# Kernel tuning notes

Measured on AMD Instinct MI355X. Metric: run time of the kernel, lower is better.

Reference implementation:

```python
import jax, jax.numpy as jnp
import numpy as np

N = 4096          # samples per domain
D_IN = 512        # input feature dim
H = 10            # hidden size of featurizer
D_OUT = 50        # featurizer output dim


def setup_inputs() -> dict:
    key = jax.random.key(0)
    ks = jax.random.split(key, 12)
    def lin(k, fan_in, fan_out):
        bound = 1.0 / np.sqrt(fan_in)
        kw, kb = jax.random.split(k)
        W = jax.random.uniform(kw, (fan_in, fan_out), jnp.float32, -bound, bound)
        b = jax.random.uniform(kb, (fan_out,), jnp.float32, -bound, bound)
        return W, b
    W1, b1 = lin(ks[0], D_IN, H)
    W2, b2 = lin(ks[1], H, H)
    W3, b3 = lin(ks[2], H, H)
    W4, b4 = lin(ks[3], H, D_OUT)
    Xs = jax.random.normal(ks[4], (N, D_IN), jnp.float32)
    Xt = jax.random.normal(ks[5], (N, D_IN), jnp.float32) + 0.1
    # epsilonOPT = log(rand(1) * 1e-10)
    epsilonOPT = jnp.log(jax.random.uniform(ks[6], (1,), jnp.float32) * 1e-10)
    sigmaOPT = jnp.sqrt(jnp.asarray(2.0 * 32 * 32, jnp.float32))
    sigma0OPT = jnp.sqrt(jnp.asarray(0.005, jnp.float32))
    return {"Xs": Xs, "Xt": Xt, "W1": W1, "b1": b1, "W2": W2, "b2": b2,
            "W3": W3, "b3": b3, "W4": W4, "b4": b4,
            "epsilonOPT": epsilonOPT, "sigmaOPT": sigmaOPT, "sigma0OPT": sigma0OPT}


def _pdist2(x, y):
    # squared pairwise distances, clamped at 0 (as in Pdist2)
    xn = jnp.sum(x * x, axis=1)[:, None]
    yn = jnp.sum(y * y, axis=1)[None, :]
    d = xn + yn - 2.0 * (x @ y.T)
    return jnp.maximum(d, 0.0)


def _featurize(x, W1, b1, W2, b2, W3, b3, W4, b4):
    sp = jax.nn.softplus
    h = sp(x @ W1 + b1)
    h = sp(h @ W2 + b2)
    h = sp(h @ W3 + b3)
    return h @ W4 + b4


def _deep_kernel(Dd, Do, ep, sigma, sigma0):
    # (1-ep)*exp(-Dd/sigma0 - Do/sigma) + ep*exp(-Do/sigma)   (L=1)
    e_org = jnp.exp(-Do / sigma)
    return (1.0 - ep) * jnp.exp(-Dd / sigma0) * e_org + ep * e_org


def reference(Xs, Xt, W1, b1, W2, b2, W3, b3, W4, b4, epsilonOPT, sigmaOPT, sigma0OPT):
    n = Xs.shape[0]
    Fea_org = jnp.concatenate([Xs, Xt], axis=0)
    Fea = _featurize(Fea_org, W1, b1, W2, b2, W3, b3, W4, b4)

    ep = jax.nn.sigmoid(epsilonOPT)[0]
    sigma = sigmaOPT ** 2
    sigma0 = sigma0OPT ** 2

    X, Y = Fea[:n], Fea[n:]
    Xo, Yo = Fea_org[:n], Fea_org[n:]

    Kx = _deep_kernel(_pdist2(X, X), _pdist2(Xo, Xo), ep, sigma, sigma0)
    Ky = _deep_kernel(_pdist2(Y, Y), _pdist2(Yo, Yo), ep, sigma, sigma0)
    Kxy = _deep_kernel(_pdist2(X, Y), _pdist2(Xo, Yo), ep, sigma, sigma0)

    nx = n
    ny = Fea.shape[0] - n
    # unbiased estimator with use_1sample_U=True
    xx = (jnp.sum(Kx) - jnp.trace(Kx)) / (nx * (nx - 1))
    yy = (jnp.sum(Ky) - jnp.trace(Ky)) / (ny * (ny - 1))
    xy = (jnp.sum(Kxy) - jnp.trace(Kxy)) / (nx * (ny - 1))
    mmd2 = xx - 2.0 * xy + yy
    return mmd2
```

## Files before the change

### kernel.cpp

```cpp
#include <hip/hip_runtime.h>
#include <math.h>

#define NHALF 4096
#define NTOT  8192
#define DIN   512
#define DFR   50
#define FPS   160
#define BM    128
#define NBI   64
#define NTRI  2080
#define T64STRIDE 524288
#define KCSTRIDE  65536

typedef short short8 __attribute__((ext_vector_type(8)));
typedef float f32x4 __attribute__((ext_vector_type(4)));

__device__ __forceinline__ float softplus_f(float x) {
    return fmaxf(x, 0.f) + log1pf(expf(-fabsf(x)));
}

__device__ __forceinline__ unsigned cvt_pk_bf16(float lo, float hi) {
    unsigned r;
    asm("v_cvt_pk_bf16_f32 %0, %1, %2" : "=v"(r) : "v"(lo), "v"(hi));
    return r;
}

__device__ __forceinline__ unsigned short bf16_rne(float v) {
    return (unsigned short)(cvt_pk_bf16(v, 0.f) & 0xffffu);
}

__device__ __forceinline__ float bf16_to_f(unsigned short s) {
    union { unsigned u; float f; } c;
    c.u = (unsigned)s << 16;
    return c.f;
}

__device__ __forceinline__ void gload_lds16(const void* g, void* l) {
    __builtin_amdgcn_global_load_lds(
        (const __attribute__((address_space(1))) void*)g,
        (__attribute__((address_space(3))) void*)l, 16, 0, 0);
}

__global__ __launch_bounds__(256) void featurize_kernel(
    const float* __restrict__ Xs, const float* __restrict__ Xt,
    const float* __restrict__ W1, const float* __restrict__ b1,
    const float* __restrict__ W2, const float* __restrict__ b2,
    const float* __restrict__ W3, const float* __restrict__ b3,
    const float* __restrict__ W4, const float* __restrict__ b4,
    const float* __restrict__ sigP, const float* __restrict__ sig0P,
    unsigned short* __restrict__ FpkA, unsigned short* __restrict__ FpkB,
    float* __restrict__ normC, char* __restrict__ Xb8)
{
    __shared__ float W1L[80 * 65];
    __shared__ __align__(16) unsigned short pkA[4][FPS];
    __shared__ __align__(16) unsigned short pkB[4][FPS];
    int tid = threadIdx.x;
    for (int e = tid; e < 5120; e += 256) {
        int r = e / 10, j = e - 10 * r;
        W1L[((r & 7) * 10 + j) * 65 + (r >> 3)] = W1[e];
    }
    __syncthreads();

    int row  = (blockIdx.x * blockDim.x + tid) >> 6;
    int lane = tid & 63, wv = tid >> 6;
    float alpha8 = 64.f / sigP[0];
    float beta   = 64.f / sig0P[0];
    const float* src = (row < NHALF) ? (Xs + (size_t)row * DIN)
                                     : (Xt + (size_t)(row - NHALF) * DIN);
    float4 v0 = ((const float4*)src)[lane * 2];
    float4 v1 = ((const float4*)src)[lane * 2 + 1];
    float x[8] = {v0.x, v0.y, v0.z, v0.w, v1.x, v1.y, v1.z, v1.w};

    float z[8];
#pragma unroll
    for (int t = 0; t < 8; ++t) z[t] = x[t] * alpha8;
    unsigned w0 = 0, w1 = 0;
    w0 = __builtin_amdgcn_cvt_pk_fp8_f32(z[0], z[1], w0, false);
    w0 = __builtin_amdgcn_cvt_pk_fp8_f32(z[2], z[3], w0, true);
    w1 = __builtin_amdgcn_cvt_pk_fp8_f32(z[4], z[5], w1, false);
    w1 = __builtin_amdgcn_cvt_pk_fp8_f32(z[6], z[7], w1, true);
    float on = 0.f, qf;
    qf = __builtin_amdgcn_cvt_f32_fp8(w0, 0); on = fmaf(qf, qf, on);
    qf = __builtin_amdgcn_cvt_f32_fp8(w0, 1); on = fmaf(qf, qf, on);
    qf = __builtin_amdgcn_cvt_f32_fp8(w0, 2); on = fmaf(qf, qf, on);
    qf = __builtin_amdgcn_cvt_f32_fp8(w0, 3); on = fmaf(qf, qf, on);
    qf = __builtin_amdgcn_cvt_f32_fp8(w1, 0); on = fmaf(qf, qf, on);
    qf = __builtin_amdgcn_cvt_f32_fp8(w1, 1); on = fmaf(qf, qf, on);
    qf = __builtin_amdgcn_cvt_f32_fp8(w1, 2); on = fmaf(qf, qf, on);
    qf = __builtin_amdgcn_cvt_f32_fp8(w1, 3); on = fmaf(qf, qf, on);
    *(uint2*)(Xb8 + (lane >> 3) * T64STRIDE + (lane & 7) * KCSTRIDE
              + (size_t)row * 8) = make_uint2(w0, w1);

    float p[10];
#pragma unroll
    for (int j = 0; j < 10; ++j) p[j] = 0.f;
#pragma unroll
    for (int t = 0; t < 8; ++t) {
        float xv = x[t];
#pragma unroll
        for (int j = 0; j < 10; ++j)
            p[j] = fmaf(xv, W1L[(t * 10 + j) * 65 + lane], p[j]);
    }
#pragma unroll
    for (int m = 32; m >= 1; m >>= 1) {
#pragma unroll
        for (int j = 0; j < 10; ++j) p[j] += __shfl_xor(p[j], m, 64);
        on += __shfl_xor(on, m, 64);
    }
    int lane10 = lane % 10;
    float pown = p[0];
#pragma unroll
    for (int j = 1; j < 10; ++j) pown = (lane10 == j) ? p[j] : pown;
    float hown = softplus_f(pown + b1[lane10]);
    float h1b[10];
#pragma unroll
    for (int k = 0; k < 10; ++k) h1b[k] = __shfl(hown, k, 64);

    float a2 = b2[lane10];
#pragma unroll
    for (int k = 0; k < 10; ++k) a2 = fmaf(h1b[k], W2[k * 10 + lane10], a2);
    float h2own = softplus_f(a2);
    float h2b[10];
#pragma unroll
    for (int k = 0; k < 10; ++k) h2b[k] = __shfl(h2own, k, 64);

    float a3 = b3[lane10];
#pragma unroll
    for (int k = 0; k < 10; ++k) a3 = fmaf(h2b[k], W3[k * 10 + lane10], a3);
    float h3own = softplus_f(a3);
    float h3b[10];
#pragma unroll
    for (int k = 0; k < 10; ++k) h3b[k] = __shfl(h3own, k, 64);

    float o = 0.f;
    if (lane < DFR) {
        float a = b4[lane];
#pragma unroll
        for (int k = 0; k < 10; ++k) a = fmaf(h3b[k], W4[k * 50 + lane], a);
        o = a;
    }
    float f = o * beta;
    unsigned short hi_s = bf16_rne(f);
    unsigned short lo_s = bf16_rne(f - bf16_to_f(hi_s));
    if (lane < DFR) {
        pkA[wv][lane] = hi_s;  pkA[wv][50 + lane] = hi_s;  pkA[wv][100 + lane] = lo_s;
        pkB[wv][lane] = hi_s;  pkB[wv][50 + lane] = lo_s;  pkB[wv][100 + lane] = hi_s;
    } else if (lane < 60) {
        pkA[wv][100 + lane] = 0;
        pkB[wv][100 + lane] = 0;
    }
    __syncthreads();
    if (lane < 20)
        *(uint4*)(FpkA + (size_t)row * FPS + lane * 8) = *(const uint4*)&pkA[wv][lane * 8];
    else if (lane < 40)
        *(uint4*)(FpkB + (size_t)row * FPS + (lane - 20) * 8) = *(const uint4*)&pkB[wv][(lane - 20) * 8];

    float fn = f * f;
#pragma unroll
    for (int m = 32; m >= 1; m >>= 1) fn += __shfl_xor(fn, m, 64);
    if (lane == 0) normC[row] = (on + fn) * (1.f / 4096.f);
}

__global__ __launch_bounds__(256, 3) void pairwise_kernel(
    const char* __restrict__ Xb8,
    const unsigned short* __restrict__ FpkA,
    const unsigned short* __restrict__ FpkB,
    const float* __restrict__ normC,
    double* __restrict__ partialsC)
{
    __shared__ char smem[49152] __attribute__((aligned(128)));
    __shared__ double sredC[4];

    int bid = blockIdx.x;
    int bi = (int)((129.0 - sqrt(16641.0 - 8.0 * (double)bid)) * 0.5);
    while (NBI * (bi + 1) - (bi + 1) * bi / 2 <= bid) ++bi;
    while (NBI * bi - bi * (bi - 1) / 2 > bid) --bi;
    int bj = bi + (bid - (NBI * bi - bi * (bi - 1) / 2));

    int tid = threadIdx.x;
    int lane = tid & 63, wave = tid >> 6;
    int g = lane >> 4, l15 = lane & 15;
    int i0w = (wave >> 1) * 64;
    int j0w = (wave & 1) * 64;
    int ri = bi * BM, rj = bj * BM;

    const char* sA8 = Xb8 + wave * KCSTRIDE + (size_t)(ri + 2 * lane) * 8;
    const char* sB8 = Xb8 + wave * KCSTRIDE + (size_t)(rj + 2 * lane) * 8;
    int srow = tid >> 2;
    int schunk = (tid & 3) ^ ((srow >> 1) & 3);
    const char* fA0 = (const char*)(FpkA + (size_t)(ri + srow) * FPS) + schunk * 16;
    const char* fB0 = (const char*)(FpkB + (size_t)(rj + srow) * FPS) + schunk * 16;
    char* lwave = (char*)smem + wave * 1024;

    int xoffA = (lane >> 4) * 1024 + (i0w + l15) * 8;
    int xoffB = 8192 + (lane >> 4) * 1024 + (j0w + l15) * 8;
    int swz = (l15 >> 1) & 3;
    int offA = (i0w + l15) * 32 + (g ^ swz) * 8;
    int offB = (j0w + l15) * 32 + (g ^ swz) * 8;

    f32x4 acc[4][4];
#pragma unroll
    for (int a = 0; a < 4; ++a)
#pragma unroll
        for (int b = 0; b < 4; ++b) acc[a][b] = (f32x4){0.f, 0.f, 0.f, 0.f};

#define STAGE8(kt, buf)                                              \
    do {                                                             \
        char* ld_ = lwave + (buf) * 16384;                           \
        const char* a_ = sA8 + (kt) * T64STRIDE;                     \
        const char* b_ = sB8 + (kt) * T64STRIDE;                     \
        gload_lds16(a_,              ld_);                           \
        gload_lds16(a_ + 4 * KCSTRIDE, ld_ + 4096);                  \
        gload_lds16(b_,              ld_ + 8192);                    \
        gload_lds16(b_ + 4 * KCSTRIDE, ld_ + 12288);                 \
    } while (0)

#define STAGEF(kf, buf)                                              \
    do {                                                             \
        char* ld_ = lwave + (buf) * 16384;                           \
        const char* gA_ = fA0 + (kf) * 64;                           \
        const char* gB_ = fB0 + (kf) * 64;                           \
        gload_lds16(gA_,         ld_);                               \
        gload_lds16(gA_ + 20480, ld_ + 4096);                        \
        gload_lds16(gB_,         ld_ + 8192);                        \
        gload_lds16(gB_ + 20480, ld_ + 12288);                       \
    } while (0)

#define COMPUTE8(buf)                                                              \
    do {                                                                           \
        const char* tc_ = smem + (buf) * 16384;                                    \
        _Pragma("unroll")                                                          \
        for (int h = 0; h < 2; ++h) {                                              \
            long a8_[4], b8_[4];                                                   \
            _Pragma("unroll")                                                      \
            for (int a = 0; a < 4; ++a)                                            \
                a8_[a] = *(const long*)(tc_ + xoffA + h * 4096 + a * 128);         \
            _Pragma("unroll")                                                      \
            for (int b = 0; b < 4; ++b)                                            \
                b8_[b] = *(const long*)(tc_ + xoffB + h * 4096 + b * 128);         \
            _Pragma("unroll")                                                      \
            for (int a = 0; a < 4; ++a)                                            \
                _Pragma("unroll")                                                  \
                for (int b = 0; b < 4; ++b)                                        \
                    acc[a][b] = __builtin_amdgcn_mfma_f32_16x16x32_fp8_fp8(        \
                        a8_[a], b8_[b], acc[a][b], 0, 0, 0);                       \
        }                                                                          \
    } while (0)

#define COMPUTE16(buf)                                                             \
    do {                                                                           \
        const unsigned short* tc_ = (const unsigned short*)(smem + (buf) * 16384); \
        short8 af_[4], bf_[4];                                                     \
        _Pragma("unroll")                                                          \
        for (int a = 0; a < 4; ++a)                                                \
            af_[a] = *(const short8*)(tc_ + offA + a * 512);                       \
        _Pragma("unroll")                                                          \
        for (int b = 0; b < 4; ++b)                                                \
            bf_[b] = *(const short8*)(tc_ + 4096 + offB + b * 512);                \
        _Pragma("unroll")                                                          \
        for (int a = 0; a < 4; ++a)                                                \
            _Pragma("unroll")                                                      \
            for (int b = 0; b < 4; ++b)                                            \
                acc[a][b] = __builtin_amdgcn_mfma_f32_16x16x32_bf16(               \
                    af_[a], bf_[b], acc[a][b], 0, 0, 0);                           \
    } while (0)

#define WAITV(N) do { asm volatile("s_waitcnt vmcnt(" #N ")" ::: "memory");        \
                      __builtin_amdgcn_sched_barrier(0); } while (0)
#define BARR1    do { __builtin_amdgcn_s_barrier();                                \
                      __builtin_amdgcn_sched_barrier(0); } while (0)
#define BARR2    do { __builtin_amdgcn_sched_barrier(0);                           \
                      asm volatile("s_waitcnt lgkmcnt(0)" ::: "memory");           \
                      __builtin_amdgcn_sched_barrier(0);                           \
                      __builtin_amdgcn_s_barrier();                                \
                      __builtin_amdgcn_sched_barrier(0); } while (0)

    STAGE8(0, 0);
    STAGE8(1, 1);
    STAGE8(2, 2);

    for (int kk = 0; kk < 8; ++kk) {
        WAITV(8);
        BARR1;
        COMPUTE8(kk % 3);
        BARR2;
        int kt = kk + 3;
        if (kt < 8) STAGE8(kt, kk % 3);
        else        STAGEF(kt - 8, kk % 3);
    }
    WAITV(8); BARR1; COMPUTE16(2); BARR2; STAGEF(3, 2);
    WAITV(8); BARR1; COMPUTE16(0); BARR2; STAGEF(4, 0);
    WAITV(8); BARR1; COMPUTE16(1);
    WAITV(4); BARR1; COMPUTE16(2);
    WAITV(0); BARR1; COMPUTE16(0);

    float nci[16], ncj[4];
#pragma unroll
    for (int a = 0; a < 4; ++a)
#pragma unroll
        for (int r = 0; r < 4; ++r)
            nci[a * 4 + r] = normC[ri + i0w + 16 * a + 4 * g + r];
#pragma unroll
    for (int b = 0; b < 4; ++b)
        ncj[b] = normC[rj + j0w + 16 * b + l15];

    float sgn = ((ri < NHALF) == (rj < NHALF)) ? 1.f : -1.f;
    float wsgn = 2.f * sgn;
    const float cf = 2.f / 4096.f;

    float locf = 0.f;
#pragma unroll
    for (int a = 0; a < 4; ++a)
#pragma unroll
        for (int b = 0; b < 4; ++b)
#pragma unroll
            for (int r = 0; r < 4; ++r) {
                int gi = ri + i0w + 16 * a + 4 * g + r;
                int gj = rj + j0w + 16 * b + l15;
                float Dc = fmaxf(fmaf(-cf, acc[a][b][r], nci[a * 4 + r] + ncj[b]), 0.f);
                float K = __expf(-Dc);
                float w = (gj > gi && gj != gi + NHALF) ? wsgn : 0.f;
                locf = fmaf(w, K, locf);
            }
    double loc = (double)locf;
#pragma unroll
    for (int m = 32; m >= 1; m >>= 1) loc += __shfl_xor(loc, m, 64);
    if (lane == 0) sredC[wave] = loc;
    __syncthreads();
    if (tid == 0)
        partialsC[bid] = sredC[0] + sredC[1] + sredC[2] + sredC[3];
#undef STAGE8
#undef STAGEF
#undef COMPUTE8
#undef COMPUTE16
#undef WAITV
#undef BARR1
#undef BARR2
}

__global__ __launch_bounds__(256) void reduce_kernel(
    const double* __restrict__ partialsC, float* __restrict__ out)
{
    double s = 0.0;
    for (int i = threadIdx.x; i < NTRI; i += 256) s += partialsC[i];
#pragma unroll
    for (int m = 32; m >= 1; m >>= 1) s += __shfl_xor(s, m, 64);
    __shared__ double ss[4];
    int w = threadIdx.x >> 6;
    if ((threadIdx.x & 63) == 0) ss[w] = s;
    __syncthreads();
    if (threadIdx.x == 0) {
        double S = ss[0] + ss[1] + ss[2] + ss[3];
        out[0] = (float)(S / (4096.0 * 4095.0));
    }
}

extern "C" void kernel_launch(void* const* d_in, const int* in_sizes, int n_in,
                              void* d_out, int out_size, void* d_ws, size_t ws_size,
                              hipStream_t stream)
{
    const float* Xs  = (const float*)d_in[0];
    const float* Xt  = (const float*)d_in[1];
    const float* W1  = (const float*)d_in[2];
    const float* b1  = (const float*)d_in[3];
    const float* W2  = (const float*)d_in[4];
    const float* b2  = (const float*)d_in[5];
    const float* W3  = (const float*)d_in[6];
    const float* b3  = (const float*)d_in[7];
    const float* W4  = (const float*)d_in[8];
    const float* b4  = (const float*)d_in[9];
    const float* sigP  = (const float*)d_in[11];
    const float* sig0P = (const float*)d_in[12];
    float* out = (float*)d_out;

    char* ws = (char*)d_ws;
    char* Xb8 = ws;
    unsigned short* FpkA = (unsigned short*)(ws + 8 * T64STRIDE);
    unsigned short* FpkB = FpkA + (size_t)NTOT * FPS;
    float* normC = (float*)(FpkB + (size_t)NTOT * FPS);
    double* partialsC = (double*)(normC + NTOT);

    featurize_kernel<<<dim3(2048), dim3(256), 0, stream>>>(
        Xs, Xt, W1, b1, W2, b2, W3, b3, W4, b4, sigP, sig0P,
        FpkA, FpkB, normC, Xb8);
    pairwise_kernel<<<dim3(NTRI), dim3(256), 0, stream>>>(
        Xb8, FpkA, FpkB, normC, partialsC);
    reduce_kernel<<<dim3(1), dim3(256), 0, stream>>>(partialsC, out);
}
```

Measured before the change: 67.68 us.

## Use 16x16x128 scaled FP8 MFMA over two staged tiles and raise wave priority

The FP8 Gram phase now uses the MI355X 16x16x128 scaled f8f6f4 MFMA in place of the 16x16x32 fp8 MFMA, pulling two LDS stage buffers per compute step. This halves the number of barrier-separated steps and issues fewer MFMAs per K chunk. The pipeline schedule is rearranged to stage two tiles after each step, and s_setprio brackets the MFMA loops. The featurizer hidden layers are also recomputed redundantly per lane instead of distributed with shuffles. The buffer rotation and lane-to-K mapping are intricate, and deeper per-step loads add register pressure.

```diff
diff --git a/kernel.cpp b/kernel.cpp
--- a/kernel.cpp
+++ b/kernel.cpp
@@ -14,6 +14,7 @@
 
 typedef short short8 __attribute__((ext_vector_type(8)));
 typedef float f32x4 __attribute__((ext_vector_type(4)));
+typedef int   i32x8 __attribute__((ext_vector_type(8)));
 
 __device__ __forceinline__ float softplus_f(float x) {
     return fmaxf(x, 0.f) + log1pf(expf(-fabsf(x)));
@@ -107,36 +108,28 @@
         for (int j = 0; j < 10; ++j) p[j] += __shfl_xor(p[j], m, 64);
         on += __shfl_xor(on, m, 64);
     }
-    int lane10 = lane % 10;
-    float pown = p[0];
-#pragma unroll
-    for (int j = 1; j < 10; ++j) pown = (lane10 == j) ? p[j] : pown;
-    float hown = softplus_f(pown + b1[lane10]);
-    float h1b[10];
-#pragma unroll
-    for (int k = 0; k < 10; ++k) h1b[k] = __shfl(hown, k, 64);
-
-    float a2 = b2[lane10];
-#pragma unroll
-    for (int k = 0; k < 10; ++k) a2 = fmaf(h1b[k], W2[k * 10 + lane10], a2);
-    float h2own = softplus_f(a2);
-    float h2b[10];
-#pragma unroll
-    for (int k = 0; k < 10; ++k) h2b[k] = __shfl(h2own, k, 64);
-
-    float a3 = b3[lane10];
-#pragma unroll
-    for (int k = 0; k < 10; ++k) a3 = fmaf(h2b[k], W3[k * 10 + lane10], a3);
-    float h3own = softplus_f(a3);
-    float h3b[10];
-#pragma unroll
-    for (int k = 0; k < 10; ++k) h3b[k] = __shfl(h3own, k, 64);
-
+    float h[10], h2[10];
+#pragma unroll
+    for (int j = 0; j < 10; ++j) h[j] = softplus_f(p[j] + b1[j]);
+#pragma unroll
+    for (int j = 0; j < 10; ++j) {
+        float a = b2[j];
+#pragma unroll
+        for (int k = 0; k < 10; ++k) a = fmaf(h[k], W2[k * 10 + j], a);
+        h2[j] = softplus_f(a);
+    }
+#pragma unroll
+    for (int j = 0; j < 10; ++j) {
+        float a = b3[j];
+#pragma unroll
+        for (int k = 0; k < 10; ++k) a = fmaf(h2[k], W3[k * 10 + j], a);
+        h[j] = softplus_f(a);
+    }
     float o = 0.f;
     if (lane < DFR) {
         float a = b4[lane];
 #pragma unroll
-        for (int k = 0; k < 10; ++k) a = fmaf(h3b[k], W4[k * 50 + lane], a);
+        for (int k = 0; k < 10; ++k) a = fmaf(h[k], W4[k * 50 + lane], a);
         o = a;
     }
     float f = o * beta;
@@ -192,8 +185,6 @@
     const char* fB0 = (const char*)(FpkB + (size_t)(rj + srow) * FPS) + schunk * 16;
     char* lwave = (char*)smem + wave * 1024;
 
-    int xoffA = (lane >> 4) * 1024 + (i0w + l15) * 8;
-    int xoffB = 8192 + (lane >> 4) * 1024 + (j0w + l15) * 8;
     int swz = (l15 >> 1) & 3;
     int offA = (i0w + l15) * 32 + (g ^ swz) * 8;
     int offB = (j0w + l15) * 32 + (g ^ swz) * 8;
@@ -209,9 +200,9 @@
         char* ld_ = lwave + (buf) * 16384;                           \
         const char* a_ = sA8 + (kt) * T64STRIDE;                     \
         const char* b_ = sB8 + (kt) * T64STRIDE;                     \
-        gload_lds16(a_,              ld_);                           \
+        gload_lds16(a_,                ld_);                         \
         gload_lds16(a_ + 4 * KCSTRIDE, ld_ + 4096);                  \
-        gload_lds16(b_,              ld_ + 8192);                    \
+        gload_lds16(b_,                ld_ + 8192);                  \
         gload_lds16(b_ + 4 * KCSTRIDE, ld_ + 12288);                 \
     } while (0)
 
@@ -226,28 +217,43 @@
         gload_lds16(gB_ + 20480, ld_ + 12288);                       \
     } while (0)
 
-#define COMPUTE8(buf)                                                              \
+#define C128(pa, pb)                                                               \
     do {                                                                           \
-        const char* tc_ = smem + (buf) * 16384;                                    \
-        _Pragma("unroll")                                                          \
-        for (int h = 0; h < 2; ++h) {                                              \
-            long a8_[4], b8_[4];                                                   \
+        const char* slA_ = smem + (((lane & 32) ? (pb) : (pa)) * 16384);           \
+        int kcb_ = ((lane >> 4) & 1) << 2;                                         \
+        const char* baseA_ = slA_ + kcb_ * 1024 + (i0w + l15) * 8;                 \
+        const char* baseB_ = slA_ + 8192 + kcb_ * 1024 + (j0w + l15) * 8;          \
+        i32x8 af_[4];                                                              \
+        _Pragma("unroll")                                                          \
+        for (int a = 0; a < 4; ++a) {                                              \
+            const char* p_ = baseA_ + a * 128;                                     \
+            uint2 t0 = *(const uint2*)(p_);                                        \
+            uint2 t1 = *(const uint2*)(p_ + 1024);                                 \
+            uint2 t2 = *(const uint2*)(p_ + 2048);                                 \
+            uint2 t3 = *(const uint2*)(p_ + 3072);                                 \
+            af_[a] = (i32x8){(int)t0.x, (int)t0.y, (int)t1.x, (int)t1.y,           \
+                             (int)t2.x, (int)t2.y, (int)t3.x, (int)t3.y};          \
+        }                                                                          \
+        __builtin_amdgcn_s_setprio(1);                                             \
+        _Pragma("unroll")                                                          \
+        for (int b = 0; b < 4; ++b) {                                              \
+            const char* p_ = baseB_ + b * 128;                                     \
+            uint2 t0 = *(const uint2*)(p_);                                        \
+            uint2 t1 = *(const uint2*)(p_ + 1024);                                 \
+            uint2 t2 = *(const uint2*)(p_ + 2048);                                 \
+            uint2 t3 = *(const uint2*)(p_ + 3072);                                 \
+            i32x8 bf_ = (i32x8){(int)t0.x, (int)t0.y, (int)t1.x, (int)t1.y,        \
+                                (int)t2.x, (int)t2.y, (int)t3.x, (int)t3.y};       \
             _Pragma("unroll")                                                      \
             for (int a = 0; a < 4; ++a)                                            \
-                a8_[a] = *(const long*)(tc_ + xoffA + h * 4096 + a * 128);         \
-            _Pragma("unroll")                                                      \
-            for (int b = 0; b < 4; ++b)                                            \
-                b8_[b] = *(const long*)(tc_ + xoffB + h * 4096 + b * 128);         \
-            _Pragma("unroll")                                                      \
-            for (int a = 0; a < 4; ++a)                                            \
-                _Pragma("unroll")                                                  \
-                for (int b = 0; b < 4; ++b)                                        \
-                    acc[a][b] = __builtin_amdgcn_mfma_f32_16x16x32_fp8_fp8(        \
-                        a8_[a], b8_[b], acc[a][b], 0, 0, 0);                       \
+                acc[a][b] = __builtin_amdgcn_mfma_scale_f32_16x16x128_f8f6f4(      \
+                    af_[a], bf_, acc[a][b], 0, 0,                                  \
+                    0, 0x7f7f7f7f, 0, 0x7f7f7f7f);                                 \
         }                                                                          \
+        __builtin_amdgcn_s_setprio(0);                                             \
     } while (0)
 
-#define COMPUTE16(buf)                                                             \
+#define C16(buf)                                                                   \
     do {                                                                           \
         const unsigned short* tc_ = (const unsigned short*)(smem + (buf) * 16384); \
         short8 af_[4], bf_[4];                                                     \
@@ -257,12 +263,14 @@
         _Pragma("unroll")                                                          \
         for (int b = 0; b < 4; ++b)                                                \
             bf_[b] = *(const short8*)(tc_ + 4096 + offB + b * 512);                \
+        __builtin_amdgcn_s_setprio(1);                                             \
         _Pragma("unroll")                                                          \
         for (int a = 0; a < 4; ++a)                                                \
             _Pragma("unroll")                                                      \
             for (int b = 0; b < 4; ++b)                                            \
                 acc[a][b] = __builtin_amdgcn_mfma_f32_16x16x32_bf16(               \
                     af_[a], bf_[b], acc[a][b], 0, 0, 0);                           \
+        __builtin_amdgcn_s_setprio(0);                                             \
     } while (0)
 
 #define WAITV(N) do { asm volatile("s_waitcnt vmcnt(" #N ")" ::: "memory");        \
@@ -275,24 +283,16 @@
                       __builtin_amdgcn_s_barrier();                                \
                       __builtin_amdgcn_sched_barrier(0); } while (0)
 
-    STAGE8(0, 0);
-    STAGE8(1, 1);
-    STAGE8(2, 2);
-
-    for (int kk = 0; kk < 8; ++kk) {
-        WAITV(8);
-        BARR1;
-        COMPUTE8(kk % 3);
-        BARR2;
-        int kt = kk + 3;
-        if (kt < 8) STAGE8(kt, kk % 3);
-        else        STAGEF(kt - 8, kk % 3);
-    }
-    WAITV(8); BARR1; COMPUTE16(2); BARR2; STAGEF(3, 2);
-    WAITV(8); BARR1; COMPUTE16(0); BARR2; STAGEF(4, 0);
-    WAITV(8); BARR1; COMPUTE16(1);
-    WAITV(4); BARR1; COMPUTE16(2);
-    WAITV(0); BARR1; COMPUTE16(0);
+    STAGE8(0, 0); STAGE8(1, 1); STAGE8(2, 2);
+    WAITV(4); BARR1; C128(0, 1); BARR2; STAGE8(3, 0); STAGE8(4, 1);
+    WAITV(4); BARR1; C128(2, 0); BARR2; STAGE8(5, 2); STAGE8(6, 0);
+    WAITV(4); BARR1; C128(1, 2); BARR2; STAGE8(7, 1); STAGEF(0, 2);
+    WAITV(4); BARR1; C128(0, 1); BARR2; STAGEF(1, 0); STAGEF(2, 1);
+    WAITV(8); BARR1; C16(2); BARR2; STAGEF(3, 2);
+    WAITV(8); BARR1; C16(0); BARR2; STAGEF(4, 0);
+    WAITV(8); BARR1; C16(1);
+    WAITV(4); BARR1; C16(2);
+    WAITV(0); BARR1; C16(0);
 
     float nci[16], ncj[4];
 #pragma unroll
@@ -331,8 +331,8 @@
         partialsC[bid] = sredC[0] + sredC[1] + sredC[2] + sredC[3];
 #undef STAGE8
 #undef STAGEF
-#undef COMPUTE8
-#undef COMPUTE16
+#undef C128
+#undef C16
 #undef WAITV
 #undef BARR1
 #undef BARR2
```

Result: slower. 109.0 us (+61.0%).
